# Kernel tuning notes

Measured on AMD Instinct MI355X. Metric: run time of the kernel, lower is better.

Reference implementation:

```python
import jax, jax.numpy as jnp
import numpy as np

B, T, C = 2, 2048, 1024
H, HS = 16, 64
FF = 4 * C
EPS = 1e-5


def _layernorm(x, w):
    mu = jnp.mean(x, axis=-1, keepdims=True)
    var = jnp.var(x, axis=-1, keepdims=True)
    return (x - mu) / jnp.sqrt(var + EPS) * w


def setup_inputs() -> dict:
    key = jax.random.key(0)
    ks = jax.random.split(key, 16)
    s_in = 1.0 / np.sqrt(C)
    s_o = 1.0 / np.sqrt(H * HS)
    s_ff = 1.0 / np.sqrt(FF)
    return {
        "x": jax.random.normal(ks[0], (B, T, C), dtype=jnp.float32),
        "ln1_w": jnp.ones((C,), jnp.float32),
        "Wq": jax.random.uniform(ks[1], (H, C, HS), jnp.float32, -s_in, s_in),
        "bq": jax.random.uniform(ks[2], (H, HS), jnp.float32, -s_in, s_in),
        "Wk": jax.random.uniform(ks[3], (H, C, HS), jnp.float32, -s_in, s_in),
        "bk": jax.random.uniform(ks[4], (H, HS), jnp.float32, -s_in, s_in),
        "Wv": jax.random.uniform(ks[5], (H, C, HS), jnp.float32, -s_in, s_in),
        "bv": jax.random.uniform(ks[6], (H, HS), jnp.float32, -s_in, s_in),
        "Wo": jax.random.uniform(ks[7], (H * HS, C), jnp.float32, -s_o, s_o),
        "bo": jax.random.uniform(ks[8], (C,), jnp.float32, -s_o, s_o),
        "ln2_w": jnp.ones((C,), jnp.float32),
        "W1": jax.random.uniform(ks[9], (C, FF), jnp.float32, -s_in, s_in),
        "b1": jax.random.uniform(ks[10], (FF,), jnp.float32, -s_in, s_in),
        "W2": jax.random.uniform(ks[11], (FF, C), jnp.float32, -s_ff, s_ff),
        "b2": jax.random.uniform(ks[12], (C,), jnp.float32, -s_ff, s_ff),
    }


def reference(x, ln1_w, Wq, bq, Wk, bk, Wv, bv, Wo, bo, ln2_w, W1, b1, W2, b2):
    h = _layernorm(x, ln1_w)                                   # [B,T,C]
    q = jnp.einsum("btc,hcd->bhtd", h, Wq) + bq[:, None, :]    # [B,H,T,HS]
    k = jnp.einsum("btc,hcd->bhtd", h, Wk) + bk[:, None, :]
    v = jnp.einsum("btc,hcd->bhtd", h, Wv) + bv[:, None, :]
    scores = jnp.einsum("bhid,bhjd->bhij", q, k) * (HS ** -0.5)
    causal = jnp.tril(jnp.ones((T, T), bool))                  # tril mask
    scores = jnp.where(causal, scores, -jnp.inf)
    # NOTE: original applies softmax over torch dim=1 of [B,T,T] = query axis i
    w = jax.nn.softmax(scores, axis=2)                         # [B,H,i,j]
    att = jnp.einsum("bhij,bhjd->bhid", w, v)                  # [B,H,T,HS]
    att = att.transpose(0, 2, 1, 3).reshape(B, T, H * HS)      # concat heads
    att = att @ Wo + bo                                        # [B,T,C]
    x1 = x + att
    h2 = _layernorm(x1, ln2_w)
    ff = jax.nn.relu(h2 @ W1 + b1) @ W2 + b2
    return x1 + ff
```

## Files before the change

kernel.cpp:

```cpp
#include <hip/hip_runtime.h>
#include <hip/hip_bf16.h>
#include <stddef.h>
#include <stdint.h>


constexpr int Bn = 2, Tn = 2048, Cn = 1024, Hn = 16, HSn = 64, FFn = 4096;
constexpr int Mn = Bn * Tn;
constexpr float EPSf = 1e-5f;
constexpr float S2 = 0.125f * 1.44269504088896340736f;

using short8 = __attribute__((ext_vector_type(8))) short;
using f32x4  = __attribute__((ext_vector_type(4))) float;
using s16x4  = __attribute__((ext_vector_type(4))) short;

#define DEVINL __device__ __forceinline__

DEVINL unsigned short f2bf(float f) {
  unsigned int u = __float_as_uint(f);
  u += 0x7fffu + ((u >> 16) & 1u);
  return (unsigned short)(u >> 16);
}

#define GLDS16(g, l) __builtin_amdgcn_global_load_lds(                        \
    (const __attribute__((address_space(1))) void*)(g),                       \
    (__attribute__((address_space(3))) void*)(l), 16, 0, 0)

__global__ __launch_bounds__(256)
void transpose_cvt(const float* __restrict__ in, unsigned short* __restrict__ out,
                   int R, int S, long zin, long zout) {
  __shared__ float tile[32][33];
  const int c0 = blockIdx.x * 32;
  const int r0 = blockIdx.y * 32;
  in  += (size_t)blockIdx.z * zin;
  out += (size_t)blockIdx.z * zout;
  const int tid = threadIdx.x;
#pragma unroll
  for (int j = 0; j < 4; ++j) {
    const int f = tid + j * 256;
    tile[f >> 5][f & 31] = in[(size_t)(r0 + (f >> 5)) * S + c0 + (f & 31)];
  }
  __syncthreads();
#pragma unroll
  for (int j = 0; j < 4; ++j) {
    const int f = tid + j * 256;
    const int sr = f >> 5, rc = f & 31;
    out[(size_t)(c0 + sr) * R + r0 + rc] = f2bf(tile[rc][sr]);
  }
}

__global__ __launch_bounds__(256)
void ln_bf16(const float* __restrict__ x, const float* __restrict__ w,
             unsigned short* __restrict__ out) {
  const int row = blockIdx.x, tid = threadIdx.x;
  const float4 v = ((const float4*)(x + (size_t)row * Cn))[tid];
  float s  = v.x + v.y + v.z + v.w;
  float ss = v.x*v.x + v.y*v.y + v.z*v.z + v.w*v.w;
#pragma unroll
  for (int o = 32; o > 0; o >>= 1) { s += __shfl_xor(s, o); ss += __shfl_xor(ss, o); }
  __shared__ float red[8];
  if ((tid & 63) == 0) { red[tid >> 6] = s; red[(tid >> 6) + 4] = ss; }
  __syncthreads();
  s  = red[0] + red[1] + red[2] + red[3];
  ss = red[4] + red[5] + red[6] + red[7];
  const float mu   = s * (1.0f / Cn);
  const float rstd = rsqrtf(ss * (1.0f / Cn) - mu * mu + EPSf);
  const float4 wv = ((const float4*)w)[tid];
  s16x4 o;
  o[0] = (short)f2bf((v.x - mu) * rstd * wv.x);
  o[1] = (short)f2bf((v.y - mu) * rstd * wv.y);
  o[2] = (short)f2bf((v.z - mu) * rstd * wv.z);
  o[3] = (short)f2bf((v.w - mu) * rstd * wv.w);
  ((s16x4*)(out + (size_t)row * Cn))[tid] = o;
}

__global__ __launch_bounds__(256)
void init_out(const float* __restrict__ b2, const float* __restrict__ x1,
              float* __restrict__ out) {
  const int idx = blockIdx.x * 256 + threadIdx.x;
  const float4 xv = ((const float4*)x1)[idx];
  const float4 bb = ((const float4*)b2)[idx & 255];
  float4 o;
  o.x = xv.x + bb.x; o.y = xv.y + bb.y; o.z = xv.z + bb.z; o.w = xv.w + bb.w;
  ((float4*)out)[idx] = o;
}

template <int EPI, int OMODE, int PIPE>
__global__ __launch_bounds__(256)
void gemm_bf16(const unsigned short* __restrict__ A,
               const unsigned short* __restrict__ Bt,
               const float* __restrict__ bias, const float* __restrict__ res,
               void* __restrict__ outp, int M, int N, int K) {
  __shared__ unsigned short As[PIPE + 1][128][64];
  __shared__ unsigned short Bs[PIPE + 1][128][64];
  const int tid = threadIdx.x;
  const int w = tid >> 6, l = tid & 63;
  const int wm = w >> 1, wn = w & 1;
  const int gx = gridDim.x, nwg = gx * gridDim.y;
  int wg = blockIdx.y * gx + blockIdx.x;
  {
    const int q = nwg >> 3, r = nwg & 7;
    const int xcd = wg & 7, off = wg >> 3;
    wg = (xcd < r ? xcd * (q + 1) : r * (q + 1) + (xcd - r) * q) + off;
  }
  const int m0 = (wg / gx) * 128, n0 = (wg % gx) * 128;
  const int kpb = K / gridDim.z;
  const int kbase = blockIdx.z * kpb;

  f32x4 acc[4][4];
#pragma unroll
  for (int i = 0; i < 4; ++i)
#pragma unroll
    for (int j = 0; j < 4; ++j) acc[i][j] = (f32x4){0.f, 0.f, 0.f, 0.f};

  const unsigned short* Abase = A + (size_t)m0 * K + kbase;
  const unsigned short* Bbase = Bt + (size_t)n0 * K + kbase;

  auto STAGE = [&](unsigned short* as, unsigned short* bs, int k0) {
#pragma unroll
    for (int j = 0; j < 4; ++j) {
      const int chunk = (w * 4 + j) * 64 + l;
      const int row = chunk >> 3, slot = chunk & 7;
      const size_t go = (size_t)row * K + k0 + ((slot ^ (row & 7)) << 3);
      GLDS16(Abase + go, as + (size_t)(w * 4 + j) * 512);
      GLDS16(Bbase + go, bs + (size_t)(w * 4 + j) * 512);
    }
  };
  auto COMPUTE = [&](const unsigned short (*as)[64], const unsigned short (*bs)[64]) {
#pragma unroll
    for (int kk = 0; kk < 2; ++kk) {
      short8 a[4], b[4];
#pragma unroll
      for (int i = 0; i < 4; ++i) {
        const int ar = wm * 64 + i * 16 + (l & 15);
        a[i] = *(const short8*)&as[ar][(((l >> 4) + kk * 4) ^ (ar & 7)) << 3];
        const int br = wn * 64 + i * 16 + (l & 15);
        b[i] = *(const short8*)&bs[br][(((l >> 4) + kk * 4) ^ (br & 7)) << 3];
      }
#pragma unroll
      for (int mi = 0; mi < 4; ++mi)
#pragma unroll
        for (int ni = 0; ni < 4; ++ni)
          acc[mi][ni] = __builtin_amdgcn_mfma_f32_16x16x32_bf16(
              a[mi], b[ni], acc[mi][ni], 0, 0, 0);
    }
  };

  const int nt = kpb >> 6;
  if (PIPE == 1) {
    STAGE(&As[0][0][0], &Bs[0][0][0], 0);
    __syncthreads();
    for (int t = 0; t + 2 < nt; t += 2) {
      STAGE(&As[1][0][0], &Bs[1][0][0], (t + 1) << 6);
      COMPUTE(As[0], Bs[0]);
      __syncthreads();
      STAGE(&As[0][0][0], &Bs[0][0][0], (t + 2) << 6);
      COMPUTE(As[1], Bs[1]);
      __syncthreads();
    }
    STAGE(&As[1][0][0], &Bs[1][0][0], (nt - 1) << 6);
    COMPUTE(As[0], Bs[0]);
    __syncthreads();
    COMPUTE(As[1], Bs[1]);
  } else {
    for (int t = 0; t < nt; ++t) {
      if (t) __syncthreads();
      STAGE(&As[0][0][0], &Bs[0][0][0], t << 6);
      __syncthreads();
      COMPUTE(As[0], Bs[0]);
    }
  }

  if (OMODE == 3) {
    if (n0 < 2048) {
      unsigned short* qk = (unsigned short*)outp;
#pragma unroll
      for (int mi = 0; mi < 4; ++mi)
#pragma unroll
        for (int ni = 0; ni < 4; ++ni) {
          const int n = n0 + wn * 64 + ni * 16 + (l & 15);
          const float bv = bias[n];
#pragma unroll
          for (int r = 0; r < 4; ++r) {
            const int m = m0 + wm * 64 + mi * 16 + ((l >> 4) << 2) + r;
            qk[(size_t)m * 2048 + n] = f2bf(acc[mi][ni][r] + bv);
          }
        }
    } else {
      unsigned short* vT = (unsigned short*)outp + (size_t)Mn * 2048;
#pragma unroll
      for (int mi = 0; mi < 4; ++mi)
#pragma unroll
        for (int ni = 0; ni < 4; ++ni) {
          const int n = n0 + wn * 64 + ni * 16 + (l & 15);
          const int nl = n - 2048;
          const int mbase = m0 + wm * 64 + mi * 16 + ((l >> 4) << 2);
          const int bb = mbase >> 11, t = mbase & 2047;
          const float bv = bias[n];
          unsigned short* dst = vT + ((size_t)(bb * 1024 + nl)) * Tn + t;
          unsigned int p0 = (unsigned)f2bf(acc[mi][ni][0] + bv) |
                            ((unsigned)f2bf(acc[mi][ni][1] + bv) << 16);
          unsigned int p1 = (unsigned)f2bf(acc[mi][ni][2] + bv) |
                            ((unsigned)f2bf(acc[mi][ni][3] + bv) << 16);
          *(unsigned int*)dst       = p0;
          *(unsigned int*)(dst + 2) = p1;
        }
    }
  } else {
#pragma unroll
    for (int mi = 0; mi < 4; ++mi)
#pragma unroll
      for (int ni = 0; ni < 4; ++ni) {
        const int n = n0 + wn * 64 + ni * 16 + (l & 15);
        const float bv = (EPI == 3) ? 0.f : bias[n];
#pragma unroll
        for (int r = 0; r < 4; ++r) {
          const int m = m0 + wm * 64 + mi * 16 + ((l >> 4) << 2) + r;
          if (EPI == 3) {
            unsafeAtomicAdd(&((float*)outp)[(size_t)m * N + n], acc[mi][ni][r]);
          } else {
            float v = acc[mi][ni][r] + bv;
            if (EPI == 1) v = fmaxf(v, 0.f);
            if (EPI == 2) v += res[(size_t)m * N + n];
            if (OMODE == 1) ((unsigned short*)outp)[(size_t)m * N + n] = f2bf(v);
            else            ((float*)outp)[(size_t)m * N + n] = v;
          }
        }
      }
  }
}

DEVINL void stage64s(unsigned short* lds, const unsigned short* g, int grs,
                     int w, int l) {
#pragma unroll
  for (int j = 0; j < 2; ++j) {
    const int chunk = (w * 2 + j) * 64 + l;
    const int row = chunk >> 3, slot = chunk & 7;
    GLDS16(g + (size_t)row * grs + ((slot ^ (row & 7)) << 3),
           lds + (size_t)(w * 2 + j) * 512);
  }
}

__global__ __launch_bounds__(256)
void colstats_mfma(const unsigned short* __restrict__ qk,
                   float* __restrict__ m2buf, float* __restrict__ rlbuf) {
  __shared__ unsigned short Ks[64][64];
  __shared__ unsigned short Qs[64][64];
  __shared__ float redm[4][4][16], redl[4][4][16];
  const int bx = blockIdx.x;
  const int bh = blockIdx.y, b = bh >> 4, h = bh & 15;
  const int tid = threadIdx.x, w = tid >> 6, l = tid & 63;
  const unsigned short* qbase = qk + ((size_t)(b * Tn)) * 2048 + h * 64;

  for (int half = 0; half < 2; ++half) {
    const int jt = half ? (31 - bx) : bx;
    const int j0 = jt * 64;
    const unsigned short* kbase = qk + ((size_t)(b * Tn + j0)) * 2048 + 1024 + h * 64;
    stage64s(&Ks[0][0], kbase, 2048, w, l);
    float m2[4], ls[4];
#pragma unroll
    for (int ni = 0; ni < 4; ++ni) { m2[ni] = -1e30f; ls[ni] = 0.f; }

    for (int i0 = j0; i0 < Tn; i0 += 64) {
      __syncthreads();
      stage64s(&Qs[0][0], qbase + (size_t)i0 * 2048, 2048, w, l);
      __syncthreads();
      f32x4 s[4];
#pragma unroll
      for (int ni = 0; ni < 4; ++ni) s[ni] = (f32x4){0.f, 0.f, 0.f, 0.f};
#pragma unroll
      for (int kk = 0; kk < 2; ++kk) {
        const int ar = w * 16 + (l & 15);
        const short8 af = *(const short8*)&Qs[ar][(((l >> 4) + kk * 4) ^ (ar & 7)) << 3];
#pragma unroll
        for (int ni = 0; ni < 4; ++ni) {
          const int br = ni * 16 + (l & 15);
          const short8 bfr = *(const short8*)&Ks[br][(((l >> 4) + kk * 4) ^ (br & 7)) << 3];
          s[ni] = __builtin_amdgcn_mfma_f32_16x16x32_bf16(af, bfr, s[ni], 0, 0, 0);
        }
      }
      const bool diag = (i0 == j0);
      const int ib = w * 16 + ((l >> 4) << 2);
#pragma unroll
      for (int ni = 0; ni < 4; ++ni) {
        const int jl = ni * 16 + (l & 15);
        float v0 = s[ni][0] * S2, v1 = s[ni][1] * S2, v2 = s[ni][2] * S2, v3 = s[ni][3] * S2;
        if (!diag) {
          const float tmax = fmaxf(fmaxf(v0, v1), fmaxf(v2, v3));
          const float mn = fmaxf(m2[ni], tmax);
          ls[ni] = ls[ni] * exp2f(m2[ni] - mn) +
                   exp2f(v0 - mn) + exp2f(v1 - mn) + exp2f(v2 - mn) + exp2f(v3 - mn);
          m2[ni] = mn;
        } else {
          const bool g0 = (ib + 0 >= jl), g1 = (ib + 1 >= jl), g2 = (ib + 2 >= jl), g3 = (ib + 3 >= jl);
          const float t0 = g0 ? v0 : -1e30f, t1 = g1 ? v1 : -1e30f;
          const float t2 = g2 ? v2 : -1e30f, t3 = g3 ? v3 : -1e30f;
          const float tmax = fmaxf(fmaxf(t0, t1), fmaxf(t2, t3));
          const float mn = fmaxf(m2[ni], tmax);
          const float e0 = g0 ? exp2f(v0 - mn) : 0.f;
          const float e1 = g1 ? exp2f(v1 - mn) : 0.f;
          const float e2 = g2 ? exp2f(v2 - mn) : 0.f;
          const float e3 = g3 ? exp2f(v3 - mn) : 0.f;
          ls[ni] = ls[ni] * exp2f(m2[ni] - mn) + e0 + e1 + e2 + e3;
          m2[ni] = mn;
        }
      }
    }
#pragma unroll
    for (int ni = 0; ni < 4; ++ni) {
#pragma unroll
      for (int off = 16; off < 64; off <<= 1) {
        const float mo = __shfl_xor(m2[ni], off);
        const float lo = __shfl_xor(ls[ni], off);
        const float mn = fmaxf(m2[ni], mo);
        ls[ni] = ls[ni] * exp2f(m2[ni] - mn) + lo * exp2f(mo - mn);
        m2[ni] = mn;
      }
    }
    if (l < 16) {
#pragma unroll
      for (int ni = 0; ni < 4; ++ni) { redm[w][ni][l] = m2[ni]; redl[w][ni][l] = ls[ni]; }
    }
    __syncthreads();
    if (tid < 64) {
      const int ni = tid >> 4, jl = tid & 15;
      float m = redm[0][ni][jl], sl = redl[0][ni][jl];
#pragma unroll
      for (int wv = 1; wv < 4; ++wv) {
        const float mo = redm[wv][ni][jl], lo = redl[wv][ni][jl];
        const float mn = fmaxf(m, mo);
        sl = sl * exp2f(m - mn) + lo * exp2f(mo - mn);
        m = mn;
      }
      m2buf[(size_t)bh * Tn + j0 + ni * 16 + jl] = m;
      rlbuf[(size_t)bh * Tn + j0 + ni * 16 + jl] = 1.0f / sl;
    }
    __syncthreads();
  }
}

__global__ __launch_bounds__(256)
void pv_mfma(const unsigned short* __restrict__ qk,
             const unsigned short* __restrict__ vT,
             const float* __restrict__ m2buf, const float* __restrict__ rlbuf,
             unsigned short* __restrict__ att) {
  __shared__ unsigned short Qs[64][64];
  __shared__ unsigned short Ks[64][64];
  __shared__ unsigned short Vs[64][64];
  __shared__ unsigned short Ps[64][64];
  __shared__ float m2s[64], rls[64];
  const int bx = blockIdx.x;
  const int bh = blockIdx.y, b = bh >> 4, h = bh & 15;
  const int tid = threadIdx.x, w = tid >> 6, l = tid & 63;
  const unsigned short* kbase = qk + ((size_t)(b * Tn)) * 2048 + 1024 + h * 64;
  const unsigned short* vbase = vT + ((size_t)(b * 1024 + h * 64)) * Tn;

  for (int half = 0; half < 2; ++half) {
    const int it = half ? (31 - bx) : bx;
    const int i0 = it * 64;
    const unsigned short* qbase = qk + ((size_t)(b * Tn + i0)) * 2048 + h * 64;
    __syncthreads();
    stage64s(&Qs[0][0], qbase, 2048, w, l);
    f32x4 oacc[4];
#pragma unroll
    for (int ni = 0; ni < 4; ++ni) oacc[ni] = (f32x4){0.f, 0.f, 0.f, 0.f};

    for (int j0 = 0; j0 <= i0; j0 += 64) {
      __syncthreads();
      stage64s(&Ks[0][0], kbase + (size_t)j0 * 2048, 2048, w, l);
#pragma unroll
      for (int j = 0; j < 2; ++j) {
        const int chunk = (w * 2 + j) * 64 + l;
        const int row = chunk >> 3, slot = chunk & 7;
        GLDS16(vbase + (size_t)row * Tn + j0 + ((slot ^ (row & 7)) << 3),
               &Vs[0][0] + (size_t)(w * 2 + j) * 512);
      }
      if (tid < 64) {
        m2s[tid] = m2buf[(size_t)bh * Tn + j0 + tid];
        rls[tid] = rlbuf[(size_t)bh * Tn + j0 + tid];
      }
      __syncthreads();
      f32x4 s[4];
#pragma unroll
      for (int ni = 0; ni < 4; ++ni) s[ni] = (f32x4){0.f, 0.f, 0.f, 0.f};
#pragma unroll
      for (int kk = 0; kk < 2; ++kk) {
        const int ar = w * 16 + (l & 15);
        const short8 af = *(const short8*)&Qs[ar][(((l >> 4) + kk * 4) ^ (ar & 7)) << 3];
#pragma unroll
        for (int ni = 0; ni < 4; ++ni) {
          const int br = ni * 16 + (l & 15);
          const short8 bfr = *(const short8*)&Ks[br][(((l >> 4) + kk * 4) ^ (br & 7)) << 3];
          s[ni] = __builtin_amdgcn_mfma_f32_16x16x32_bf16(af, bfr, s[ni], 0, 0, 0);
        }
      }
      const bool diag = (j0 == i0);
      const int ib = w * 16 + ((l >> 4) << 2);
      unsigned short* Pf = &Ps[0][0];
#pragma unroll
      for (int ni = 0; ni < 4; ++ni) {
        const int jl = ni * 16 + (l & 15);
        const float mj = m2s[jl], rj = rls[jl];
#pragma unroll
        for (int r = 0; r < 4; ++r) {
          float p = exp2f(s[ni][r] * S2 - mj) * rj;
          if (diag && (ib + r < jl)) p = 0.f;
          const int il = ib + r;
          Pf[il * 64 + (((jl >> 3) ^ (il & 7)) << 3) + (jl & 7)] = f2bf(p);
        }
      }
#pragma unroll
      for (int kk = 0; kk < 2; ++kk) {
        const int ar = w * 16 + (l & 15);
        const short8 pf = *(const short8*)&Ps[ar][(((l >> 4) + kk * 4) ^ (ar & 7)) << 3];
#pragma unroll
        for (int ni = 0; ni < 4; ++ni) {
          const int br = ni * 16 + (l & 15);
          const short8 vf = *(const short8*)&Vs[br][(((l >> 4) + kk * 4) ^ (br & 7)) << 3];
          oacc[ni] = __builtin_amdgcn_mfma_f32_16x16x32_bf16(pf, vf, oacc[ni], 0, 0, 0);
        }
      }
    }
#pragma unroll
    for (int ni = 0; ni < 4; ++ni) {
      const int col = h * 64 + ni * 16 + (l & 15);
#pragma unroll
      for (int r = 0; r < 4; ++r) {
        const int m = b * Tn + i0 + w * 16 + ((l >> 4) << 2) + r;
        att[(size_t)m * 1024 + col] = f2bf(oacc[ni][r]);
      }
    }
  }
}

extern "C" void kernel_launch(void* const* d_in, const int* in_sizes, int n_in,
                              void* d_out, int out_size, void* d_ws, size_t ws_size,
                              hipStream_t stream) {
  const float* x    = (const float*)d_in[0];
  const float* ln1w = (const float*)d_in[1];
  const float* Wq   = (const float*)d_in[2];
  const float* bq   = (const float*)d_in[3];
  const float* Wk   = (const float*)d_in[4];
  const float* bk   = (const float*)d_in[5];
  const float* Wv   = (const float*)d_in[6];
  const float* bv   = (const float*)d_in[7];
  const float* Wo   = (const float*)d_in[8];
  const float* bo   = (const float*)d_in[9];
  const float* ln2w = (const float*)d_in[10];
  const float* W1   = (const float*)d_in[11];
  const float* b1   = (const float*)d_in[12];
  const float* W2   = (const float*)d_in[13];
  const float* b2   = (const float*)d_in[14];

  uint8_t* wsb = (uint8_t*)d_ws;
  unsigned short* h     = (unsigned short*)(wsb);
  unsigned short* qkb   = (unsigned short*)(wsb + (8ull  << 20));
  unsigned short* vT    = (unsigned short*)(wsb + (24ull << 20));
  unsigned short* attb  = (unsigned short*)(wsb + (32ull << 20));
  float*          x1    = (float*)         (wsb + (40ull << 20));
  unsigned short* ffmid = qkb;
  unsigned short* Wqkvt = (unsigned short*)(wsb + (56ull << 20));
  unsigned short* Wot   = (unsigned short*)(wsb + (62ull << 20));
  unsigned short* W1t   = (unsigned short*)(wsb + (64ull << 20));
  unsigned short* W2t   = (unsigned short*)(wsb + (72ull << 20));
  float*          biasqkv=(float*)         (wsb + (80ull << 20));
  float*          m2buf = (float*)         (wsb + (81ull << 20));
  float*          rlbuf = (float*)         (wsb + (81ull << 20) + (256ull << 10));

  transpose_cvt<<<dim3(2, 32, 16), 256, 0, stream>>>(Wq, Wqkvt,                  1024, 64, 65536, 65536);
  transpose_cvt<<<dim3(2, 32, 16), 256, 0, stream>>>(Wk, Wqkvt + 1024 * 1024,    1024, 64, 65536, 65536);
  transpose_cvt<<<dim3(2, 32, 16), 256, 0, stream>>>(Wv, Wqkvt + 2 * 1024 * 1024, 1024, 64, 65536, 65536);
  transpose_cvt<<<dim3(32, 32, 1), 256, 0, stream>>>(Wo, Wot,  1024, 1024, 0, 0);
  transpose_cvt<<<dim3(128, 32, 1), 256, 0, stream>>>(W1, W1t, 1024, 4096, 0, 0);
  transpose_cvt<<<dim3(32, 128, 1), 256, 0, stream>>>(W2, W2t, 4096, 1024, 0, 0);
  hipMemcpyAsync(biasqkv,        bq, 1024 * sizeof(float), hipMemcpyDeviceToDevice, stream);
  hipMemcpyAsync(biasqkv + 1024, bk, 1024 * sizeof(float), hipMemcpyDeviceToDevice, stream);
  hipMemcpyAsync(biasqkv + 2048, bv, 1024 * sizeof(float), hipMemcpyDeviceToDevice, stream);

  ln_bf16<<<Mn, 256, 0, stream>>>(x, ln1w, h);
  gemm_bf16<0, 3, 0><<<dim3(24, 32), 256, 0, stream>>>(h, Wqkvt, biasqkv, nullptr, qkb, Mn, 3072, Cn);
  colstats_mfma<<<dim3(16, Bn * Hn), 256, 0, stream>>>(qkb, m2buf, rlbuf);
  pv_mfma<<<dim3(16, Bn * Hn), 256, 0, stream>>>(qkb, vT, m2buf, rlbuf, attb);
  gemm_bf16<2, 0, 1><<<dim3(8, 32), 256, 0, stream>>>(attb, Wot, bo, x, x1, Mn, 1024, Cn);
  ln_bf16<<<Mn, 256, 0, stream>>>(x1, ln2w, h);
  gemm_bf16<1, 1, 0><<<dim3(32, 32), 256, 0, stream>>>(h, W1t, b1, nullptr, ffmid, Mn, FFn, Cn);
  init_out<<<Mn * Cn / 1024, 256, 0, stream>>>(b2, x1, (float*)d_out);
  gemm_bf16<3, 0, 1><<<dim3(8, 32, 2), 256, 0, stream>>>(ffmid, W2t, nullptr, nullptr, (float*)d_out, Mn, Cn, FFn);
}
```

Before: 423.0 us.

## Split-K the output projection with atomics and drop GEMM double buffering

The attention output projection now uses split-K across two slices with atomic accumulation into a buffer pre-initialised with bias plus residual, replacing its fused bias/residual epilogue. The FFN down-projection split-K is raised from two to four slices. The double-buffered (PIPE=1) GEMM path is removed, so every GEMM uses a single-buffered LDS tile with a sync per K step. This trades less overlap of loads and compute and more atomic traffic for more workgroups on the narrow N=1024 GEMMs.

```diff
diff --git a/kernel.cpp b/kernel.cpp
--- a/kernel.cpp
+++ b/kernel.cpp
@@ -74,24 +74,24 @@
 }
 
 __global__ __launch_bounds__(256)
-void init_out(const float* __restrict__ b2, const float* __restrict__ x1,
-              float* __restrict__ out) {
+void init_bias_res(const float* __restrict__ bias, const float* __restrict__ res,
+                   float* __restrict__ out) {
   const int idx = blockIdx.x * 256 + threadIdx.x;
-  const float4 xv = ((const float4*)x1)[idx];
-  const float4 bb = ((const float4*)b2)[idx & 255];
+  const float4 xv = ((const float4*)res)[idx];
+  const float4 bb = ((const float4*)bias)[idx & 255];
   float4 o;
   o.x = xv.x + bb.x; o.y = xv.y + bb.y; o.z = xv.z + bb.z; o.w = xv.w + bb.w;
   ((float4*)out)[idx] = o;
 }
 
-template <int EPI, int OMODE, int PIPE>
+template <int EPI, int OMODE>
 __global__ __launch_bounds__(256)
 void gemm_bf16(const unsigned short* __restrict__ A,
                const unsigned short* __restrict__ Bt,
-               const float* __restrict__ bias, const float* __restrict__ res,
+               const float* __restrict__ bias,
                void* __restrict__ outp, int M, int N, int K) {
-  __shared__ unsigned short As[PIPE + 1][128][64];
-  __shared__ unsigned short Bs[PIPE + 1][128][64];
+  __shared__ unsigned short As[128][64];
+  __shared__ unsigned short Bs[128][64];
   const int tid = threadIdx.x;
   const int w = tid >> 6, l = tid & 63;
   const int wm = w >> 1, wn = w & 1;
@@ -115,26 +115,28 @@
   const unsigned short* Abase = A + (size_t)m0 * K + kbase;
   const unsigned short* Bbase = Bt + (size_t)n0 * K + kbase;
 
-  auto STAGE = [&](unsigned short* as, unsigned short* bs, int k0) {
+  const int nt = kpb >> 6;
+  for (int t = 0; t < nt; ++t) {
+    if (t) __syncthreads();
+    const int k0 = t << 6;
 #pragma unroll
     for (int j = 0; j < 4; ++j) {
       const int chunk = (w * 4 + j) * 64 + l;
       const int row = chunk >> 3, slot = chunk & 7;
       const size_t go = (size_t)row * K + k0 + ((slot ^ (row & 7)) << 3);
-      GLDS16(Abase + go, as + (size_t)(w * 4 + j) * 512);
-      GLDS16(Bbase + go, bs + (size_t)(w * 4 + j) * 512);
-    }
-  };
-  auto COMPUTE = [&](const unsigned short (*as)[64], const unsigned short (*bs)[64]) {
+      GLDS16(Abase + go, &As[0][0] + (size_t)(w * 4 + j) * 512);
+      GLDS16(Bbase + go, &Bs[0][0] + (size_t)(w * 4 + j) * 512);
+    }
+    __syncthreads();
 #pragma unroll
     for (int kk = 0; kk < 2; ++kk) {
       short8 a[4], b[4];
 #pragma unroll
       for (int i = 0; i < 4; ++i) {
         const int ar = wm * 64 + i * 16 + (l & 15);
-        a[i] = *(const short8*)&as[ar][(((l >> 4) + kk * 4) ^ (ar & 7)) << 3];
+        a[i] = *(const short8*)&As[ar][(((l >> 4) + kk * 4) ^ (ar & 7)) << 3];
         const int br = wn * 64 + i * 16 + (l & 15);
-        b[i] = *(const short8*)&bs[br][(((l >> 4) + kk * 4) ^ (br & 7)) << 3];
+        b[i] = *(const short8*)&Bs[br][(((l >> 4) + kk * 4) ^ (br & 7)) << 3];
       }
 #pragma unroll
       for (int mi = 0; mi < 4; ++mi)
@@ -142,31 +144,6 @@
         for (int ni = 0; ni < 4; ++ni)
           acc[mi][ni] = __builtin_amdgcn_mfma_f32_16x16x32_bf16(
               a[mi], b[ni], acc[mi][ni], 0, 0, 0);
-    }
-  };
-
-  const int nt = kpb >> 6;
-  if (PIPE == 1) {
-    STAGE(&As[0][0][0], &Bs[0][0][0], 0);
-    __syncthreads();
-    for (int t = 0; t + 2 < nt; t += 2) {
-      STAGE(&As[1][0][0], &Bs[1][0][0], (t + 1) << 6);
-      COMPUTE(As[0], Bs[0]);
-      __syncthreads();
-      STAGE(&As[0][0][0], &Bs[0][0][0], (t + 2) << 6);
-      COMPUTE(As[1], Bs[1]);
-      __syncthreads();
-    }
-    STAGE(&As[1][0][0], &Bs[1][0][0], (nt - 1) << 6);
-    COMPUTE(As[0], Bs[0]);
-    __syncthreads();
-    COMPUTE(As[1], Bs[1]);
-  } else {
-    for (int t = 0; t < nt; ++t) {
-      if (t) __syncthreads();
-      STAGE(&As[0][0][0], &Bs[0][0][0], t << 6);
-      __syncthreads();
-      COMPUTE(As[0], Bs[0]);
     }
   }
 
@@ -220,7 +197,6 @@
           } else {
             float v = acc[mi][ni][r] + bv;
             if (EPI == 1) v = fmaxf(v, 0.f);
-            if (EPI == 2) v += res[(size_t)m * N + n];
             if (OMODE == 1) ((unsigned short*)outp)[(size_t)m * N + n] = f2bf(v);
             else            ((float*)outp)[(size_t)m * N + n] = v;
           }
@@ -477,12 +453,13 @@
   hipMemcpyAsync(biasqkv + 2048, bv, 1024 * sizeof(float), hipMemcpyDeviceToDevice, stream);
 
   ln_bf16<<<Mn, 256, 0, stream>>>(x, ln1w, h);
-  gemm_bf16<0, 3, 0><<<dim3(24, 32), 256, 0, stream>>>(h, Wqkvt, biasqkv, nullptr, qkb, Mn, 3072, Cn);
+  gemm_bf16<0, 3><<<dim3(24, 32), 256, 0, stream>>>(h, Wqkvt, biasqkv, qkb, Mn, 3072, Cn);
   colstats_mfma<<<dim3(16, Bn * Hn), 256, 0, stream>>>(qkb, m2buf, rlbuf);
   pv_mfma<<<dim3(16, Bn * Hn), 256, 0, stream>>>(qkb, vT, m2buf, rlbuf, attb);
-  gemm_bf16<2, 0, 1><<<dim3(8, 32), 256, 0, stream>>>(attb, Wot, bo, x, x1, Mn, 1024, Cn);
+  init_bias_res<<<Mn * Cn / 1024, 256, 0, stream>>>(bo, x, x1);
+  gemm_bf16<3, 0><<<dim3(8, 32, 2), 256, 0, stream>>>(attb, Wot, nullptr, x1, Mn, Cn, Cn);
   ln_bf16<<<Mn, 256, 0, stream>>>(x1, ln2w, h);
-  gemm_bf16<1, 1, 0><<<dim3(32, 32), 256, 0, stream>>>(h, W1t, b1, nullptr, ffmid, Mn, FFn, Cn);
-  init_out<<<Mn * Cn / 1024, 256, 0, stream>>>(b2, x1, (float*)d_out);
-  gemm_bf16<3, 0, 1><<<dim3(8, 32, 2), 256, 0, stream>>>(ffmid, W2t, nullptr, nullptr, (float*)d_out, Mn, Cn, FFn);
-}
+  gemm_bf16<1, 1><<<dim3(32, 32), 256, 0, stream>>>(h, W1t, b1, ffmid, Mn, FFn, Cn);
+  init_bias_res<<<Mn * Cn / 1024, 256, 0, stream>>>(b2, x1, (float*)d_out);
+  gemm_bf16<3, 0><<<dim3(8, 32, 4), 256, 0, stream>>>(ffmid, W2t, nullptr, (float*)d_out, Mn, Cn, FFn);
+}
```

Measured after the change: 450.1 us. 1.06x slower.
